# Performance work log

Measured on AMD Instinct MI355X. Metric: run time of the kernel, lower is better.

The kernel has to match this reference:

```python
import jax, jax.numpy as jnp
import numpy as np

N = 100_000   # nodes
E = 600_000   # edges
D = 128       # embed_dim
G = 1000      # graphs (batch ids)
L = 3         # num_layers


def setup_inputs() -> dict:
    key = jax.random.key(0)
    ks = jax.random.split(key, 12)
    s = 1.0 / np.sqrt(D)
    return {
        "x": jax.random.normal(ks[0], (N, D), jnp.float32),
        "edge_index": jax.random.randint(ks[1], (2, E), 0, N),
        "batch": jnp.sort(jax.random.randint(ks[2], (N,), 0, G)),
        "mask": jax.random.randint(ks[3], (N,), 0, 2),
        # stacked GCNConv weights/biases (in=hidden=out=D)
        "gcn_w": jax.random.normal(ks[4], (L, D, D), jnp.float32) * s,
        "gcn_b": jnp.zeros((L, D), jnp.float32),
        # MLP head: Linear(D,D) -> ReLU -> Linear(D,1)
        "lin1_w": jax.random.normal(ks[5], (D, D), jnp.float32) * s,
        "lin1_b": jnp.zeros((D,), jnp.float32),
        "lin2_w": jax.random.normal(ks[6], (D,), jnp.float32) * s,
        "lin2_b": jnp.zeros((), jnp.float32),
    }


def gcn_forward(x, src, dst, gcn_w, gcn_b):
    # symmetric gcn_norm with self-loops: deg[i] = 1 + in-degree(i)
    deg = jax.ops.segment_sum(jnp.ones((E,), x.dtype), dst, num_segments=N) + 1.0
    dinv = jax.lax.rsqrt(deg)
    enorm = dinv[src] * dinv[dst]          # [E] edge normalization
    self_norm = (dinv * dinv)[:, None]     # [N,1] self-loop normalization
    h = x
    for l in range(L):
        h = h @ gcn_w[l]                   # [N,D]
        h = (jax.ops.segment_sum(h[src] * enorm[:, None], dst, num_segments=N)
             + h * self_norm)
        h = h + gcn_b[l]
        if l < L - 1:
            h = jax.nn.relu(h)  # (dropout inactive at inference)
    return h


def reference(x, edge_index, batch, mask, gcn_w, gcn_b, lin1_w, lin1_b, lin2_w, lin2_b):
    src, dst = edge_index[0], edge_index[1]
    h = gcn_forward(x, src, dst, gcn_w, gcn_b)
    # MLP head -> per-node score [N]
    s = jax.nn.relu(h @ lin1_w + lin1_b) @ lin2_w + lin2_b
    s = jnp.where(mask == 0, jnp.float32(-1e9), s)
    # per-graph (segment) softmax — fused replacement for the unique/batch loop
    m = jax.ops.segment_max(s, batch, num_segments=G)
    e = jnp.exp(s - m[batch])
    z = jax.ops.segment_sum(e, batch, num_segments=G)
    return e / z[batch]
```

## Files before the change

kernel.cpp:

```cpp
#include <hip/hip_runtime.h>
#include <hip/hip_bf16.h>

typedef unsigned int u32;
typedef unsigned short u16;
typedef __attribute__((ext_vector_type(8))) short bf16x8;
typedef __attribute__((ext_vector_type(4))) float f32x4;

__device__ __forceinline__ float u16tof(u16 u){ return __uint_as_float(((u32)u) << 16); }
__device__ __forceinline__ float lo16(u32 v){ return __uint_as_float(v << 16); }
__device__ __forceinline__ float hi16(u32 v){ return __uint_as_float(v & 0xffff0000u); }
__device__ __forceinline__ u16 ftobf(float f){
  u32 b = __float_as_uint(f);
  return (u16)((b + 0x7FFFu + ((b >> 16) & 1u)) >> 16);
}
__device__ __forceinline__ u32 pack2(float a, float b){
  return (u32)ftobf(a) | ((u32)ftobf(b) << 16);
}
__device__ __forceinline__ float ldf(const void* p, int i, int isbf){
  return isbf ? u16tof(((const u16*)p)[i]) : ((const float*)p)[i];
}

__device__ __forceinline__ void gather_rows(const u16* __restrict__ Tin, const int* __restrict__ eid,
                                            int j0, int b1e, int l16, float* a){
  const int last = b1e - 1;
  for (int j = j0; j < b1e; j += 8){
    int ss[8];
    #pragma unroll
    for (int k = 0; k < 8; ++k){
      const int jj = j + k;
      ss[k] = eid[jj > last ? last : jj];
    }
    uint4 vv[8];
    #pragma unroll
    for (int k = 0; k < 8; ++k){
      vv[k] = ((const uint4*)(Tin + (size_t)ss[k] * 128))[l16];
    }
    #pragma unroll
    for (int k = 0; k < 8; ++k){
      const float mk = (j + k <= last) ? 1.f : 0.f;
      a[0] = fmaf(lo16(vv[k].x), mk, a[0]);
      a[1] = fmaf(hi16(vv[k].x), mk, a[1]);
      a[2] = fmaf(lo16(vv[k].y), mk, a[2]);
      a[3] = fmaf(hi16(vv[k].y), mk, a[3]);
      a[4] = fmaf(lo16(vv[k].z), mk, a[4]);
      a[5] = fmaf(hi16(vv[k].z), mk, a[5]);
      a[6] = fmaf(lo16(vv[k].w), mk, a[6]);
      a[7] = fmaf(hi16(vv[k].w), mk, a[7]);
    }
  }
}

__global__ __launch_bounds__(256) void k_prep(const void* __restrict__ gw, const void* __restrict__ l1w,
                                              const void* __restrict__ x, u16* __restrict__ Wf,
                                              u16* __restrict__ Hb, int L, int n8, int cvtB, int goffB,
                                              const int* __restrict__ batch, int* __restrict__ goff,
                                              int N, int G,
                                              const int* __restrict__ dst, int* __restrict__ hist,
                                              int nE, int chunk, int* __restrict__ flag){
  __shared__ int sh[256];
  const int b = blockIdx.x;
  const int t = threadIdx.x;
  const int histStart = L + 1 + cvtB + goffB;

  if (b >= histStart){
    sh[t] = 0; __syncthreads();
    const int blk = b - histStart;
    const int e0 = blk * chunk, e1 = min(e0 + chunk, nE);
    for (int e = e0 + t; e < e1; e += 256) atomicAdd(&sh[dst[e] >> 9], 1);
    __syncthreads();
    hist[blk * 256 + t] = sh[t];
    return;
  }
  if (b >= L + 1 + cvtB){
    const int i = (b - (L + 1 + cvtB)) * 256 + t;
    if (i >= N) return;
    const int bt = batch[i];
    const int prev = (i == 0) ? -1 : batch[i - 1];
    for (int g = prev + 1; g <= bt; ++g) goff[g] = i;
    if (i == N - 1){ for (int g = bt + 1; g <= G; ++g) goff[g] = N; }
    return;
  }
  if (t == 0) sh[0] = 0;
  __syncthreads();
  if (b <= L){
    int local = 0;
    for (int i = t; i < 4096; i += 256){
      u32 e = (((const u32*)gw)[i] >> 7) & 0xFFu;
      if (e >= 100u && e < 127u) local++;
    }
    atomicAdd(&sh[0], local);
    __syncthreads();
    const int isbf = (sh[0] > 2048) ? 1 : 0;
    if (b == 0 && t == 0) *flag = isbf;

    const void* src = (b < L) ? gw : l1w;
    const int sbase = (b < L) ? b * 16384 : 0;
    u16* dstp = Wf + (size_t)b * 16384;
    for (int g = t; g < 2048; g += 256){
      const int tt = g >> 8, ks = (g >> 6) & 3, lane = g & 63;
      const int n = tt * 16 + (lane & 15);
      const int k0 = ks * 32 + ((lane >> 4) << 3);
      u16* d = dstp + (size_t)g * 8;
      #pragma unroll
      for (int j = 0; j < 8; ++j){
        d[j] = ftobf(ldf(src, sbase + (k0 + j) * 128 + n, isbf));
      }
    }
  } else {
    u32 e = (((const u32*)gw)[t] >> 7) & 0xFFu;
    atomicAdd(&sh[0], (e >= 100u && e < 127u) ? 1 : 0);
    __syncthreads();
    if (sh[0] > 128) return;
    const int i = (b - (L + 1)) * 256 + t;
    if (i >= n8) return;
    const float4 a = ((const float4*)x)[i * 2];
    const float4 c = ((const float4*)x)[i * 2 + 1];
    u16* o = Hb + (size_t)i * 8;
    o[0] = ftobf(a.x); o[1] = ftobf(a.y); o[2] = ftobf(a.z); o[3] = ftobf(a.w);
    o[4] = ftobf(c.x); o[5] = ftobf(c.y); o[6] = ftobf(c.z); o[7] = ftobf(c.w);
  }
}

__global__ __launch_bounds__(256) void k_hscan(int* __restrict__ hist, int* __restrict__ bb, int nE){
  const int t = threadIdx.x;
  int run = 0;
  for (int j = 0; j < 256; j += 8){
    int v[8];
    #pragma unroll
    for (int k = 0; k < 8; ++k) v[k] = hist[(j + k) * 256 + t];
    #pragma unroll
    for (int k = 0; k < 8; ++k){
      hist[(j + k) * 256 + t] = run;
      run += v[k];
    }
  }
  __shared__ int sm[256];
  sm[t] = run; __syncthreads();
  for (int off = 1; off < 256; off <<= 1){
    int a = (t >= off) ? sm[t - off] : 0;
    __syncthreads();
    sm[t] += a;
    __syncthreads();
  }
  bb[t] = sm[t] - run;
  if (t == 255) bb[256] = nE;
}

__global__ __launch_bounds__(256) void k_scatter(const int* __restrict__ src, const int* __restrict__ dst,
                                                 const int* __restrict__ hist, const int* __restrict__ bb,
                                                 int2* __restrict__ tmpe, int nE, int chunk){
  __shared__ int base[256];
  const int blk = blockIdx.x, t = threadIdx.x;
  base[t] = bb[t] + hist[blk * 256 + t];
  __syncthreads();
  const int e0 = blk * chunk, e1 = min(e0 + chunk, nE);
  for (int e = e0 + t; e < e1; e += 256){
    const int d = dst[e];
    const int pos = atomicAdd(&base[d >> 9], 1);
    tmpe[pos] = make_int2(src[e], d);
  }
}

__global__ __launch_bounds__(256) void k_local(const int2* __restrict__ tmpe, const int* __restrict__ bb,
                                               int* __restrict__ boff, int* __restrict__ eid,
                                               float* __restrict__ dinv, int N, int nE, int nbkt){
  __shared__ int hcnt[512];
  __shared__ int hoff[512];
  const int b = blockIdx.x, t = threadIdx.x;
  const int n0 = b << 9;
  const int n1 = min(n0 + 512, N);
  const int nn = n1 - n0;
  const int e0 = bb[b], e1 = bb[b + 1];
  hcnt[t] = 0; hcnt[t + 256] = 0;
  __syncthreads();
  for (int e = e0 + t; e < e1; e += 256) atomicAdd(&hcnt[tmpe[e].y - n0], 1);
  __syncthreads();
  const int v0 = hcnt[t], v1 = hcnt[t + 256];
  hoff[t] = v0; hoff[t + 256] = v1;
  __syncthreads();
  for (int off = 1; off < 512; off <<= 1){
    int a0 = (t >= off) ? hoff[t - off] : 0;
    int a1 = (t + 256 >= off) ? hoff[t + 256 - off] : 0;
    __syncthreads();
    hoff[t] += a0; hoff[t + 256] += a1;
    __syncthreads();
  }
  const int ex0 = hoff[t] - v0 + e0;
  const int ex1 = hoff[t + 256] - v1 + e0;
  if (t < nn){       boff[n0 + t] = ex0;        dinv[n0 + t] = rsqrtf((float)v0 + 1.0f); }
  if (t + 256 < nn){ boff[n0 + t + 256] = ex1;  dinv[n0 + t + 256] = rsqrtf((float)v1 + 1.0f); }
  if (b == nbkt - 1 && t == 0) boff[N] = nE;
  __syncthreads();
  hoff[t] = ex0; hoff[t + 256] = ex1;
  __syncthreads();
  for (int e = e0 + t; e < e1; e += 256){
    const int2 pr = tmpe[e];
    const int pos = atomicAdd(&hoff[pr.y - n0], 1);
    eid[pos] = pr.x;
  }
}

__global__ __launch_bounds__(256) void k_mm(const void* __restrict__ X, const u16* __restrict__ Hb,
                                            const u16* __restrict__ Wf, const float* __restrict__ dinv,
                                            u16* __restrict__ T, int n, const int* __restrict__ fl){
  __shared__ u16 smw[16384];
  const int isbf = *fl;
  const u16* A = isbf ? (const u16*)X : Hb;
  {
    const uint4* s = (const uint4*)Wf;
    uint4* d = (uint4*)smw;
    for (int i = threadIdx.x; i < 2048; i += 256) d[i] = s[i];
  }
  __syncthreads();

  const int wave = threadIdx.x >> 6, lane = threadIdx.x & 63;
  const int m0 = blockIdx.x * 64 + wave * 16;
  int arow = m0 + (lane & 15); if (arow > n - 1) arow = n - 1;
  const u16* aptr = A + (size_t)arow * 128 + ((lane >> 4) << 3);

  f32x4 acc[8];
  #pragma unroll
  for (int t = 0; t < 8; ++t) acc[t] = (f32x4){0.f, 0.f, 0.f, 0.f};

  #pragma unroll
  for (int ks = 0; ks < 4; ++ks){
    const bf16x8 a = *(const bf16x8*)(aptr + ks * 32);
    #pragma unroll
    for (int t = 0; t < 8; ++t){
      const bf16x8 b = *(const bf16x8*)(smw + (size_t)(((t * 4 + ks) * 64 + lane) * 8));
      acc[t] = __builtin_amdgcn_mfma_f32_16x16x32_bf16(a, b, acc[t], 0, 0, 0);
    }
  }
  __syncthreads();

  const int quad = lane >> 4, col0 = lane & 15;
  float dv[4];
  #pragma unroll
  for (int r = 0; r < 4; ++r){
    const int row = m0 + quad * 4 + r;
    dv[r] = (row < n) ? dinv[row] : 0.f;
  }
  u16* my = smw + wave * 2112;
  #pragma unroll
  for (int t = 0; t < 8; ++t){
    #pragma unroll
    for (int r = 0; r < 4; ++r){
      my[(quad * 4 + r) * 132 + t * 16 + col0] = ftobf(acc[t][r] * dv[r]);
    }
  }
  #pragma unroll
  for (int i = 0; i < 4; ++i){
    const int row = i * 4 + (lane >> 4);
    const int grow = m0 + row;
    const int c8 = (lane & 15) * 8;
    if (grow < n){
      const u16* s = &my[row * 132 + c8];
      uint2 lo = *(const uint2*)(s);
      uint2 hi = *(const uint2*)(s + 4);
      *(uint4*)&T[(size_t)grow * 128 + c8] = make_uint4(lo.x, lo.y, hi.x, hi.y);
    }
  }
}

__global__ __launch_bounds__(256) void k_gmm(const u16* __restrict__ Tin, const int* __restrict__ boff,
                                             const int* __restrict__ eid, const float* __restrict__ dinv,
                                             const void* __restrict__ bias, int layer,
                                             const u16* __restrict__ Wf, u16* __restrict__ Tout,
                                             int n, const int* __restrict__ fl){
  __shared__ u16 sma[16 * 132];
  const int isbf = *fl;
  const int wave = threadIdx.x >> 6, lane = threadIdx.x & 63;
  const int sub = lane >> 4, l16 = lane & 15;
  const int m0 = blockIdx.x * 16;

  const int node = m0 + wave * 4 + sub;
  float h[8];
  #pragma unroll
  for (int k = 0; k < 8; ++k) h[k] = 0.f;
  if (node < n){
    const uint4 sv = ((const uint4*)(Tin + (size_t)node * 128))[l16];
    float a[8];
    a[0] = lo16(sv.x); a[1] = hi16(sv.x); a[2] = lo16(sv.y); a[3] = hi16(sv.y);
    a[4] = lo16(sv.z); a[5] = hi16(sv.z); a[6] = lo16(sv.w); a[7] = hi16(sv.w);
    gather_rows(Tin, eid, boff[node], boff[node + 1], l16, a);
    const float di = dinv[node];
    const int bb = layer * 128 + l16 * 8;
    #pragma unroll
    for (int k = 0; k < 8; ++k){
      h[k] = fmaxf(fmaf(a[k], di, ldf(bias, bb + k, isbf)), 0.f);
    }
  }
  {
    uint4 o;
    o.x = pack2(h[0], h[1]); o.y = pack2(h[2], h[3]); o.z = pack2(h[4], h[5]); o.w = pack2(h[6], h[7]);
    *(uint4*)&sma[(wave * 4 + sub) * 132 + l16 * 8] = o;
  }
  __syncthreads();

  f32x4 acc[2];
  acc[0] = (f32x4){0.f,0.f,0.f,0.f}; acc[1] = (f32x4){0.f,0.f,0.f,0.f};
  #pragma unroll
  for (int ks = 0; ks < 4; ++ks){
    const bf16x8 a = *(const bf16x8*)(sma + l16 * 132 + sub * 8 + ks * 32);
    #pragma unroll
    for (int tt = 0; tt < 2; ++tt){
      const int t = wave * 2 + tt;
      const bf16x8 b = *(const bf16x8*)(Wf + (size_t)(((t * 4 + ks) * 64 + lane) * 8));
      acc[tt] = __builtin_amdgcn_mfma_f32_16x16x32_bf16(a, b, acc[tt], 0, 0, 0);
    }
  }
  __syncthreads();

  float dv[4];
  #pragma unroll
  for (int r = 0; r < 4; ++r){
    const int row = m0 + sub * 4 + r;
    dv[r] = (row < n) ? dinv[row] : 0.f;
  }
  #pragma unroll
  for (int tt = 0; tt < 2; ++tt){
    const int t = wave * 2 + tt;
    #pragma unroll
    for (int r = 0; r < 4; ++r){
      sma[(sub * 4 + r) * 132 + t * 16 + l16] = ftobf(acc[tt][r] * dv[r]);
    }
  }
  __syncthreads();

  {
    const int row = threadIdx.x >> 4;
    const int c8 = (threadIdx.x & 15) * 8;
    if (m0 + row < n){
      const u16* s = &sma[row * 132 + c8];
      uint2 lo = *(const uint2*)(s);
      uint2 hi = *(const uint2*)(s + 4);
      *(uint4*)&Tout[(size_t)(m0 + row) * 128 + c8] = make_uint4(lo.x, lo.y, hi.x, hi.y);
    }
  }
}

__global__ __launch_bounds__(256) void k_ghead(const u16* __restrict__ Tin, const int* __restrict__ boff,
                                               const int* __restrict__ eid, const float* __restrict__ dinv,
                                               const void* __restrict__ bias, int layer,
                                               const u16* __restrict__ Wf, const void* __restrict__ b1,
                                               const void* __restrict__ w2, const void* __restrict__ b2,
                                               const int* __restrict__ mask, float* __restrict__ s,
                                               int n, const int* __restrict__ fl){
  __shared__ u16 sma[16 * 132];
  __shared__ float sred[4][16];
  const int isbf = *fl;
  const int wave = threadIdx.x >> 6, lane = threadIdx.x & 63;
  const int sub = lane >> 4, l16 = lane & 15;
  const int m0 = blockIdx.x * 16;

  const int node = m0 + wave * 4 + sub;
  float h[8];
  #pragma unroll
  for (int k = 0; k < 8; ++k) h[k] = 0.f;
  if (node < n){
    const uint4 sv = ((const uint4*)(Tin + (size_t)node * 128))[l16];
    float a[8];
    a[0] = lo16(sv.x); a[1] = hi16(sv.x); a[2] = lo16(sv.y); a[3] = hi16(sv.y);
    a[4] = lo16(sv.z); a[5] = hi16(sv.z); a[6] = lo16(sv.w); a[7] = hi16(sv.w);
    gather_rows(Tin, eid, boff[node], boff[node + 1], l16, a);
    const float di = dinv[node];
    const int bb = layer * 128 + l16 * 8;
    #pragma unroll
    for (int k = 0; k < 8; ++k){
      h[k] = fmaf(a[k], di, ldf(bias, bb + k, isbf));
    }
  }
  {
    uint4 o;
    o.x = pack2(h[0], h[1]); o.y = pack2(h[2], h[3]); o.z = pack2(h[4], h[5]); o.w = pack2(h[6], h[7]);
    *(uint4*)&sma[(wave * 4 + sub) * 132 + l16 * 8] = o;
  }
  __syncthreads();

  f32x4 acc[2];
  acc[0] = (f32x4){0.f,0.f,0.f,0.f}; acc[1] = (f32x4){0.f,0.f,0.f,0.f};
  #pragma unroll
  for (int ks = 0; ks < 4; ++ks){
    const bf16x8 a = *(const bf16x8*)(sma + l16 * 132 + sub * 8 + ks * 32);
    #pragma unroll
    for (int tt = 0; tt < 2; ++tt){
      const int t = wave * 2 + tt;
      const bf16x8 b = *(const bf16x8*)(Wf + (size_t)(((t * 4 + ks) * 64 + lane) * 8));
      acc[tt] = __builtin_amdgcn_mfma_f32_16x16x32_bf16(a, b, acc[tt], 0, 0, 0);
    }
  }

  float p0 = 0.f, p1 = 0.f, p2 = 0.f, p3 = 0.f;
  #pragma unroll
  for (int tt = 0; tt < 2; ++tt){
    const int col = (wave * 2 + tt) * 16 + l16;
    const float bv = ldf(b1, col, isbf);
    const float wv = ldf(w2, col, isbf);
    p0 = fmaf(fmaxf(acc[tt][0] + bv, 0.f), wv, p0);
    p1 = fmaf(fmaxf(acc[tt][1] + bv, 0.f), wv, p1);
    p2 = fmaf(fmaxf(acc[tt][2] + bv, 0.f), wv, p2);
    p3 = fmaf(fmaxf(acc[tt][3] + bv, 0.f), wv, p3);
  }
  #pragma unroll
  for (int k = 1; k < 16; k <<= 1){
    p0 += __shfl_xor(p0, k);
    p1 += __shfl_xor(p1, k);
    p2 += __shfl_xor(p2, k);
    p3 += __shfl_xor(p3, k);
  }
  if (l16 == 0){
    sred[wave][sub * 4 + 0] = p0;
    sred[wave][sub * 4 + 1] = p1;
    sred[wave][sub * 4 + 2] = p2;
    sred[wave][sub * 4 + 3] = p3;
  }
  __syncthreads();
  if (threadIdx.x < 16){
    const int row = m0 + threadIdx.x;
    if (row < n){
      float sc = sred[0][threadIdx.x] + sred[1][threadIdx.x] + sred[2][threadIdx.x] + sred[3][threadIdx.x]
               + ldf(b2, 0, isbf);
      if (mask[row] == 0) sc = -1e9f;
      s[row] = sc;
    }
  }
}

__global__ __launch_bounds__(256) void k_gsm(const float* __restrict__ s, const int* __restrict__ goff,
                                             void* __restrict__ out, int G, const int* __restrict__ fl){
  const int g = blockIdx.x * 4 + (threadIdx.x >> 6);
  if (g >= G) return;
  const int lane = threadIdx.x & 63;
  const int i0 = goff[g], i1 = goff[g + 1];
  if (i0 >= i1) return;
  float m = -3.4e38f;
  for (int j = i0 + lane; j < i1; j += 64) m = fmaxf(m, s[j]);
  #pragma unroll
  for (int k = 32; k; k >>= 1) m = fmaxf(m, __shfl_xor(m, k));
  float zz = 0.f;
  for (int j = i0 + lane; j < i1; j += 64) zz += expf(s[j] - m);
  #pragma unroll
  for (int k = 32; k; k >>= 1) zz += __shfl_xor(zz, k);
  const float rz = 1.f / zz;
  const int isbf = *fl;
  for (int j = i0 + lane; j < i1; j += 64){
    const float v = expf(s[j] - m) * rz;
    if (isbf) ((u16*)out)[j] = ftobf(v);
    else      ((float*)out)[j] = v;
  }
}

extern "C" void kernel_launch(void* const* d_in, const int* in_sizes, int n_in,
                              void* d_out, int out_size, void* d_ws, size_t ws_size,
                              hipStream_t stream){
  const void* x    = d_in[0];
  const int* ei    = (const int*)d_in[1];
  const int* batch = (const int*)d_in[2];
  const int* mask  = (const int*)d_in[3];
  const void* gw   = d_in[4];
  const void* gb   = d_in[5];
  const void* l1w  = d_in[6];
  const void* l1b  = d_in[7];
  const void* l2w  = d_in[8];
  const void* l2b  = d_in[9];

  const int N = in_sizes[2];
  const int E = in_sizes[1] / 2;
  const int D = 128;
  const int L = in_sizes[4] / (D * D);
  const int G = 1000;

  char* p = (char*)d_ws;
  u16*  Hb    = (u16*)p;   p += (size_t)N * D * sizeof(u16);
  u16*  Tb    = (u16*)p;   p += (size_t)N * D * sizeof(u16);
  u16*  Wf    = (u16*)p;   p += (size_t)(L + 1) * D * D * sizeof(u16);
  float* dinv = (float*)p; p += (size_t)N * sizeof(float);
  float* sbuf = (float*)p; p += (size_t)N * sizeof(float);
  int*  boff  = (int*)p;   p += (size_t)(N + 1) * sizeof(int);
  int*  eid   = (int*)p;   p += (size_t)E * sizeof(int);
  int*  goff  = (int*)p;   p += (size_t)(G + 1) * sizeof(int);
  int*  hist  = (int*)p;   p += 256 * 256 * sizeof(int);
  int*  bb    = (int*)p;   p += 260 * sizeof(int);
  int2* tmpe  = (int2*)p;  p += (size_t)E * sizeof(int2);
  int*  flag  = (int*)p;   p += 256;

  const int* srcp = ei;
  const int* dstp = ei + E;

  const int mmg   = (N + 63) / 64;
  const int fg    = (N + 15) / 16;
  const int n8    = N * D / 8;
  const int cvtB  = (n8 + 255) / 256;
  const int goffB = (N + 255) / 256;
  const int chunk = (E + 255) / 256;
  const int nbkt  = (N + 511) / 512;

  k_prep<<<(L + 1) + cvtB + goffB + 256, 256, 0, stream>>>(gw, l1w, x, Wf, Hb, L, n8, cvtB, goffB,
                                                           batch, goff, N, G, dstp, hist, E, chunk, flag);
  k_hscan<<<1, 256, 0, stream>>>(hist, bb, E);
  k_scatter<<<256, 256, 0, stream>>>(srcp, dstp, hist, bb, tmpe, E, chunk);
  k_local<<<nbkt, 256, 0, stream>>>(tmpe, bb, boff, eid, dinv, N, E, nbkt);

  k_mm<<<mmg, 256, 0, stream>>>(x, Hb, Wf, dinv, Tb, N, flag);
  k_gmm<<<fg, 256, 0, stream>>>(Tb, boff, eid, dinv, gb, 0, Wf + (size_t)1 * D * D, Hb, N, flag);
  k_gmm<<<fg, 256, 0, stream>>>(Hb, boff, eid, dinv, gb, 1, Wf + (size_t)2 * D * D, Tb, N, flag);
  k_ghead<<<fg, 256, 0, stream>>>(Tb, boff, eid, dinv, gb, 2, Wf + (size_t)L * D * D,
                                  l1b, l2w, l2b, mask, sbuf, N, flag);
  k_gsm<<<(G + 3) / 4, 256, 0, stream>>>(sbuf, goff, d_out, G, flag);
}
```

Baseline: 324.7 us.

## Stage weight matrix in LDS and widen gather-GEMM blocks to 64 rows

```diff
diff --git a/kernel.cpp b/kernel.cpp
--- a/kernel.cpp
+++ b/kernel.cpp
@@ -262,16 +262,25 @@
   }
 }
 
-__global__ __launch_bounds__(256) void k_gmm(const u16* __restrict__ Tin, const int* __restrict__ boff,
-                                             const int* __restrict__ eid, const float* __restrict__ dinv,
-                                             const void* __restrict__ bias, int layer,
-                                             const u16* __restrict__ Wf, u16* __restrict__ Tout,
-                                             int n, const int* __restrict__ fl){
-  __shared__ u16 sma[16 * 132];
+__global__ __launch_bounds__(1024, 8) void k_gmm(const u16* __restrict__ Tin, const int* __restrict__ boff,
+                                                 const int* __restrict__ eid, const float* __restrict__ dinv,
+                                                 const void* __restrict__ bias, int layer,
+                                                 const u16* __restrict__ Wf, u16* __restrict__ Tout,
+                                                 int n, const int* __restrict__ fl){
+  __shared__ u16 smw[16384];
+  __shared__ u16 sma[64 * 132];
   const int isbf = *fl;
-  const int wave = threadIdx.x >> 6, lane = threadIdx.x & 63;
+  const int tid = threadIdx.x;
+  const int wave = tid >> 6, lane = tid & 63;
   const int sub = lane >> 4, l16 = lane & 15;
-  const int m0 = blockIdx.x * 16;
+  const int m0 = blockIdx.x * 64;
+
+  {
+    const uint4* s = (const uint4*)Wf;
+    uint4* d = (uint4*)smw;
+    d[tid] = s[tid];
+    d[tid + 1024] = s[tid + 1024];
+  }
 
   const int node = m0 + wave * 4 + sub;
   float h[8];
@@ -297,15 +306,16 @@
   }
   __syncthreads();
 
+  const int rg = wave >> 2, cp = wave & 3;
   f32x4 acc[2];
   acc[0] = (f32x4){0.f,0.f,0.f,0.f}; acc[1] = (f32x4){0.f,0.f,0.f,0.f};
   #pragma unroll
   for (int ks = 0; ks < 4; ++ks){
-    const bf16x8 a = *(const bf16x8*)(sma + l16 * 132 + sub * 8 + ks * 32);
+    const bf16x8 a = *(const bf16x8*)(sma + (rg * 16 + l16) * 132 + sub * 8 + ks * 32);
     #pragma unroll
     for (int tt = 0; tt < 2; ++tt){
-      const int t = wave * 2 + tt;
-      const bf16x8 b = *(const bf16x8*)(Wf + (size_t)(((t * 4 + ks) * 64 + lane) * 8));
+      const int t = cp * 2 + tt;
+      const bf16x8 b = *(const bf16x8*)(smw + (size_t)(((t * 4 + ks) * 64 + lane) * 8));
       acc[tt] = __builtin_amdgcn_mfma_f32_16x16x32_bf16(a, b, acc[tt], 0, 0, 0);
     }
   }
@@ -314,22 +324,22 @@
   float dv[4];
   #pragma unroll
   for (int r = 0; r < 4; ++r){
-    const int row = m0 + sub * 4 + r;
+    const int row = m0 + rg * 16 + sub * 4 + r;
     dv[r] = (row < n) ? dinv[row] : 0.f;
   }
   #pragma unroll
   for (int tt = 0; tt < 2; ++tt){
-    const int t = wave * 2 + tt;
+    const int t = cp * 2 + tt;
     #pragma unroll
     for (int r = 0; r < 4; ++r){
-      sma[(sub * 4 + r) * 132 + t * 16 + l16] = ftobf(acc[tt][r] * dv[r]);
+      sma[(rg * 16 + sub * 4 + r) * 132 + t * 16 + l16] = ftobf(acc[tt][r] * dv[r]);
     }
   }
   __syncthreads();
 
   {
-    const int row = threadIdx.x >> 4;
-    const int c8 = (threadIdx.x & 15) * 8;
+    const int row = tid >> 4;
+    const int c8 = (tid & 15) * 8;
     if (m0 + row < n){
       const u16* s = &sma[row * 132 + c8];
       uint2 lo = *(const uint2*)(s);
@@ -339,19 +349,28 @@
   }
 }
 
-__global__ __launch_bounds__(256) void k_ghead(const u16* __restrict__ Tin, const int* __restrict__ boff,
-                                               const int* __restrict__ eid, const float* __restrict__ dinv,
-                                               const void* __restrict__ bias, int layer,
-                                               const u16* __restrict__ Wf, const void* __restrict__ b1,
-                                               const void* __restrict__ w2, const void* __restrict__ b2,
-                                               const int* __restrict__ mask, float* __restrict__ s,
-                                               int n, const int* __restrict__ fl){
-  __shared__ u16 sma[16 * 132];
-  __shared__ float sred[4][16];
+__global__ __launch_bounds__(1024, 8) void k_ghead(const u16* __restrict__ Tin, const int* __restrict__ boff,
+                                                   const int* __restrict__ eid, const float* __restrict__ dinv,
+                                                   const void* __restrict__ bias, int layer,
+                                                   const u16* __restrict__ Wf, const void* __restrict__ b1,
+                                                   const void* __restrict__ w2, const void* __restrict__ b2,
+                                                   const int* __restrict__ mask, float* __restrict__ s,
+                                                   int n, const int* __restrict__ fl){
+  __shared__ u16 smw[16384];
+  __shared__ u16 sma[64 * 132];
+  __shared__ float sred[16][16];
   const int isbf = *fl;
-  const int wave = threadIdx.x >> 6, lane = threadIdx.x & 63;
+  const int tid = threadIdx.x;
+  const int wave = tid >> 6, lane = tid & 63;
   const int sub = lane >> 4, l16 = lane & 15;
-  const int m0 = blockIdx.x * 16;
+  const int m0 = blockIdx.x * 64;
+
+  {
+    const uint4* sp = (const uint4*)Wf;
+    uint4* d = (uint4*)smw;
+    d[tid] = sp[tid];
+    d[tid + 1024] = sp[tid + 1024];
+  }
 
   const int node = m0 + wave * 4 + sub;
   float h[8];
@@ -377,15 +396,16 @@
   }
   __syncthreads();
 
+  const int rg = wave >> 2, cp = wave & 3;
   f32x4 acc[2];
   acc[0] = (f32x4){0.f,0.f,0.f,0.f}; acc[1] = (f32x4){0.f,0.f,0.f,0.f};
   #pragma unroll
   for (int ks = 0; ks < 4; ++ks){
-    const bf16x8 a = *(const bf16x8*)(sma + l16 * 132 + sub * 8 + ks * 32);
+    const bf16x8 a = *(const bf16x8*)(sma + (rg * 16 + l16) * 132 + sub * 8 + ks * 32);
     #pragma unroll
     for (int tt = 0; tt < 2; ++tt){
-      const int t = wave * 2 + tt;
-      const bf16x8 b = *(const bf16x8*)(Wf + (size_t)(((t * 4 + ks) * 64 + lane) * 8));
+      const int t = cp * 2 + tt;
+      const bf16x8 b = *(const bf16x8*)(smw + (size_t)(((t * 4 + ks) * 64 + lane) * 8));
       acc[tt] = __builtin_amdgcn_mfma_f32_16x16x32_bf16(a, b, acc[tt], 0, 0, 0);
     }
   }
@@ -393,7 +413,7 @@
   float p0 = 0.f, p1 = 0.f, p2 = 0.f, p3 = 0.f;
   #pragma unroll
   for (int tt = 0; tt < 2; ++tt){
-    const int col = (wave * 2 + tt) * 16 + l16;
+    const int col = (cp * 2 + tt) * 16 + l16;
     const float bv = ldf(b1, col, isbf);
     const float wv = ldf(w2, col, isbf);
     p0 = fmaf(fmaxf(acc[tt][0] + bv, 0.f), wv, p0);
@@ -415,10 +435,12 @@
     sred[wave][sub * 4 + 3] = p3;
   }
   __syncthreads();
-  if (threadIdx.x < 16){
-    const int row = m0 + threadIdx.x;
+  if (tid < 64){
+    const int row = m0 + tid;
     if (row < n){
-      float sc = sred[0][threadIdx.x] + sred[1][threadIdx.x] + sred[2][threadIdx.x] + sred[3][threadIdx.x]
+      const int rg2 = tid >> 4, idx = tid & 15;
+      float sc = sred[rg2 * 4 + 0][idx] + sred[rg2 * 4 + 1][idx]
+               + sred[rg2 * 4 + 2][idx] + sred[rg2 * 4 + 3][idx]
                + ldf(b2, 0, isbf);
       if (mask[row] == 0) sc = -1e9f;
       s[row] = sc;
@@ -488,7 +510,7 @@
   const int* dstp = ei + E;
 
   const int mmg   = (N + 63) / 64;
-  const int fg    = (N + 15) / 16;
+  const int fg    = (N + 63) / 64;
   const int n8    = N * D / 8;
   const int cvtB  = (n8 + 255) / 256;
   const int goffB = (N + 255) / 256;
@@ -502,9 +524,9 @@
   k_local<<<nbkt, 256, 0, stream>>>(tmpe, bb, boff, eid, dinv, N, E, nbkt);
 
   k_mm<<<mmg, 256, 0, stream>>>(x, Hb, Wf, dinv, Tb, N, flag);
-  k_gmm<<<fg, 256, 0, stream>>>(Tb, boff, eid, dinv, gb, 0, Wf + (size_t)1 * D * D, Hb, N, flag);
-  k_gmm<<<fg, 256, 0, stream>>>(Hb, boff, eid, dinv, gb, 1, Wf + (size_t)2 * D * D, Tb, N, flag);
-  k_ghead<<<fg, 256, 0, stream>>>(Tb, boff, eid, dinv, gb, 2, Wf + (size_t)L * D * D,
-                                  l1b, l2w, l2b, mask, sbuf, N, flag);
+  k_gmm<<<fg, 1024, 0, stream>>>(Tb, boff, eid, dinv, gb, 0, Wf + (size_t)1 * D * D, Hb, N, flag);
+  k_gmm<<<fg, 1024, 0, stream>>>(Hb, boff, eid, dinv, gb, 1, Wf + (size_t)2 * D * D, Tb, N, flag);
+  k_ghead<<<fg, 1024, 0, stream>>>(Tb, boff, eid, dinv, gb, 2, Wf + (size_t)L * D * D,
+                                   l1b, l2w, l2b, mask, sbuf, N, flag);
   k_gsm<<<(G + 3) / 4, 256, 0, stream>>>(sbuf, goff, d_out, G, flag);
 }
```

Result: slower. 532.1 us (+63.9%).

## Process two nodes per thread group and 32-row tiles in gather+matmul kernels

Applied to the files above, without the earlier changes.

```diff
diff --git a/kernel.cpp b/kernel.cpp
--- a/kernel.cpp
+++ b/kernel.cpp
@@ -20,33 +20,38 @@
   return isbf ? u16tof(((const u16*)p)[i]) : ((const float*)p)[i];
 }
 
-__device__ __forceinline__ void gather_rows(const u16* __restrict__ Tin, const int* __restrict__ eid,
-                                            int j0, int b1e, int l16, float* a){
-  const int last = b1e - 1;
-  for (int j = j0; j < b1e; j += 8){
-    int ss[8];
-    #pragma unroll
-    for (int k = 0; k < 8; ++k){
-      const int jj = j + k;
-      ss[k] = eid[jj > last ? last : jj];
-    }
-    uint4 vv[8];
-    #pragma unroll
-    for (int k = 0; k < 8; ++k){
-      vv[k] = ((const uint4*)(Tin + (size_t)ss[k] * 128))[l16];
-    }
-    #pragma unroll
-    for (int k = 0; k < 8; ++k){
-      const float mk = (j + k <= last) ? 1.f : 0.f;
-      a[0] = fmaf(lo16(vv[k].x), mk, a[0]);
-      a[1] = fmaf(hi16(vv[k].x), mk, a[1]);
-      a[2] = fmaf(lo16(vv[k].y), mk, a[2]);
-      a[3] = fmaf(hi16(vv[k].y), mk, a[3]);
-      a[4] = fmaf(lo16(vv[k].z), mk, a[4]);
-      a[5] = fmaf(hi16(vv[k].z), mk, a[5]);
-      a[6] = fmaf(lo16(vv[k].w), mk, a[6]);
-      a[7] = fmaf(hi16(vv[k].w), mk, a[7]);
-    }
+__device__ __forceinline__ void acc8(float* a, uint4 v, float mk){
+  a[0] = fmaf(lo16(v.x), mk, a[0]);
+  a[1] = fmaf(hi16(v.x), mk, a[1]);
+  a[2] = fmaf(lo16(v.y), mk, a[2]);
+  a[3] = fmaf(hi16(v.y), mk, a[3]);
+  a[4] = fmaf(lo16(v.z), mk, a[4]);
+  a[5] = fmaf(hi16(v.z), mk, a[5]);
+  a[6] = fmaf(lo16(v.w), mk, a[6]);
+  a[7] = fmaf(hi16(v.w), mk, a[7]);
+}
+
+__device__ __forceinline__ void gather2(const u16* __restrict__ Tin, const int* __restrict__ eid,
+                                        int jA, int eA, int jB, int eB, int l16,
+                                        float* a, float* b){
+  while (jA < eA || jB < eB){
+    int sA[4], sB[4];
+    #pragma unroll
+    for (int k = 0; k < 4; ++k){
+      const int iA = jA + k; sA[k] = eid[iA < eA ? iA : 0];
+      const int iB = jB + k; sB[k] = eid[iB < eB ? iB : 0];
+    }
+    uint4 vA[4], vB[4];
+    #pragma unroll
+    for (int k = 0; k < 4; ++k) vA[k] = ((const uint4*)(Tin + (size_t)sA[k] * 128))[l16];
+    #pragma unroll
+    for (int k = 0; k < 4; ++k) vB[k] = ((const uint4*)(Tin + (size_t)sB[k] * 128))[l16];
+    #pragma unroll
+    for (int k = 0; k < 4; ++k){
+      acc8(a, vA[k], (jA + k < eA) ? 1.f : 0.f);
+      acc8(b, vB[k], (jB + k < eB) ? 1.f : 0.f);
+    }
+    jA += 4; jB += 4;
   }
 }
 
@@ -267,46 +272,64 @@
                                              const void* __restrict__ bias, int layer,
                                              const u16* __restrict__ Wf, u16* __restrict__ Tout,
                                              int n, const int* __restrict__ fl){
-  __shared__ u16 sma[16 * 132];
+  __shared__ u16 sma[32 * 132];
   const int isbf = *fl;
-  const int wave = threadIdx.x >> 6, lane = threadIdx.x & 63;
+  const int tid = threadIdx.x;
+  const int wave = tid >> 6, lane = tid & 63;
   const int sub = lane >> 4, l16 = lane & 15;
-  const int m0 = blockIdx.x * 16;
-
-  const int node = m0 + wave * 4 + sub;
-  float h[8];
-  #pragma unroll
-  for (int k = 0; k < 8; ++k) h[k] = 0.f;
-  if (node < n){
-    const uint4 sv = ((const uint4*)(Tin + (size_t)node * 128))[l16];
-    float a[8];
-    a[0] = lo16(sv.x); a[1] = hi16(sv.x); a[2] = lo16(sv.y); a[3] = hi16(sv.y);
-    a[4] = lo16(sv.z); a[5] = hi16(sv.z); a[6] = lo16(sv.w); a[7] = hi16(sv.w);
-    gather_rows(Tin, eid, boff[node], boff[node + 1], l16, a);
-    const float di = dinv[node];
-    const int bb = layer * 128 + l16 * 8;
-    #pragma unroll
-    for (int k = 0; k < 8; ++k){
-      h[k] = fmaxf(fmaf(a[k], di, ldf(bias, bb + k, isbf)), 0.f);
-    }
+  const int m0 = blockIdx.x * 32;
+
+  const int nA = m0 + wave * 8 + sub;
+  const int nB = nA + 4;
+  float a[8], b[8];
+  #pragma unroll
+  for (int k = 0; k < 8; ++k){ a[k] = 0.f; b[k] = 0.f; }
+  int jA = 0, eA = 0, jB = 0, eB = 0;
+  if (nA < n){ jA = boff[nA]; eA = boff[nA + 1]; }
+  if (nB < n){ jB = boff[nB]; eB = boff[nB + 1]; }
+  if (nA < n){
+    const uint4 sv = ((const uint4*)(Tin + (size_t)nA * 128))[l16];
+    acc8(a, sv, 1.f);
+  }
+  if (nB < n){
+    const uint4 sv = ((const uint4*)(Tin + (size_t)nB * 128))[l16];
+    acc8(b, sv, 1.f);
+  }
+  gather2(Tin, eid, jA, eA, jB, eB, l16, a, b);
+
+  const int bb = layer * 128 + l16 * 8;
+  if (nA < n){
+    const float di = dinv[nA];
+    #pragma unroll
+    for (int k = 0; k < 8; ++k) a[k] = fmaxf(fmaf(a[k], di, ldf(bias, bb + k, isbf)), 0.f);
+  }
+  if (nB < n){
+    const float di = dinv[nB];
+    #pragma unroll
+    for (int k = 0; k < 8; ++k) b[k] = fmaxf(fmaf(b[k], di, ldf(bias, bb + k, isbf)), 0.f);
   }
   {
-    uint4 o;
-    o.x = pack2(h[0], h[1]); o.y = pack2(h[2], h[3]); o.z = pack2(h[4], h[5]); o.w = pack2(h[6], h[7]);
-    *(uint4*)&sma[(wave * 4 + sub) * 132 + l16 * 8] = o;
-  }
-  __syncthreads();
-
-  f32x4 acc[2];
-  acc[0] = (f32x4){0.f,0.f,0.f,0.f}; acc[1] = (f32x4){0.f,0.f,0.f,0.f};
+    uint4 oA, oB;
+    oA.x = pack2(a[0], a[1]); oA.y = pack2(a[2], a[3]); oA.z = pack2(a[4], a[5]); oA.w = pack2(a[6], a[7]);
+    oB.x = pack2(b[0], b[1]); oB.y = pack2(b[2], b[3]); oB.z = pack2(b[4], b[5]); oB.w = pack2(b[6], b[7]);
+    *(uint4*)&sma[(wave * 8 + sub) * 132 + l16 * 8] = oA;
+    *(uint4*)&sma[(wave * 8 + sub + 4) * 132 + l16 * 8] = oB;
+  }
+  __syncthreads();
+
+  const int r0 = (wave & 1) * 16;
+  const int cg = wave >> 1;
+  f32x4 acc[4];
+  #pragma unroll
+  for (int tt = 0; tt < 4; ++tt) acc[tt] = (f32x4){0.f, 0.f, 0.f, 0.f};
   #pragma unroll
   for (int ks = 0; ks < 4; ++ks){
-    const bf16x8 a = *(const bf16x8*)(sma + l16 * 132 + sub * 8 + ks * 32);
-    #pragma unroll
-    for (int tt = 0; tt < 2; ++tt){
-      const int t = wave * 2 + tt;
-      const bf16x8 b = *(const bf16x8*)(Wf + (size_t)(((t * 4 + ks) * 64 + lane) * 8));
-      acc[tt] = __builtin_amdgcn_mfma_f32_16x16x32_bf16(a, b, acc[tt], 0, 0, 0);
+    const bf16x8 av = *(const bf16x8*)(sma + (r0 + l16) * 132 + sub * 8 + ks * 32);
+    #pragma unroll
+    for (int tt = 0; tt < 4; ++tt){
+      const int t = cg * 4 + tt;
+      const bf16x8 bv = *(const bf16x8*)(Wf + (size_t)(((t * 4 + ks) * 64 + lane) * 8));
+      acc[tt] = __builtin_amdgcn_mfma_f32_16x16x32_bf16(av, bv, acc[tt], 0, 0, 0);
     }
   }
   __syncthreads();
@@ -314,22 +337,23 @@
   float dv[4];
   #pragma unroll
   for (int r = 0; r < 4; ++r){
-    const int row = m0 + sub * 4 + r;
+    const int row = m0 + r0 + sub * 4 + r;
     dv[r] = (row < n) ? dinv[row] : 0.f;
   }
   #pragma unroll
-  for (int tt = 0; tt < 2; ++tt){
-    const int t = wave * 2 + tt;
+  for (int tt = 0; tt < 4; ++tt){
     #pragma unroll
     for (int r = 0; r < 4; ++r){
-      sma[(sub * 4 + r) * 132 + t * 16 + l16] = ftobf(acc[tt][r] * dv[r]);
-    }
-  }
-  __syncthreads();
-
-  {
-    const int row = threadIdx.x >> 4;
-    const int c8 = (threadIdx.x & 15) * 8;
+      sma[(r0 + sub * 4 + r) * 132 + (cg * 4 + tt) * 16 + l16] = ftobf(acc[tt][r] * dv[r]);
+    }
+  }
+  __syncthreads();
+
+  #pragma unroll
+  for (int i = 0; i < 2; ++i){
+    const int idx = tid + i * 256;
+    const int row = idx >> 4;
+    const int c8 = (idx & 15) * 8;
     if (m0 + row < n){
       const u16* s = &sma[row * 132 + c8];
       uint2 lo = *(const uint2*)(s);
@@ -346,54 +370,72 @@
                                                const void* __restrict__ w2, const void* __restrict__ b2,
                                                const int* __restrict__ mask, float* __restrict__ s,
                                                int n, const int* __restrict__ fl){
-  __shared__ u16 sma[16 * 132];
+  __shared__ u16 sma[32 * 132];
   __shared__ float sred[4][16];
   const int isbf = *fl;
-  const int wave = threadIdx.x >> 6, lane = threadIdx.x & 63;
+  const int tid = threadIdx.x;
+  const int wave = tid >> 6, lane = tid & 63;
   const int sub = lane >> 4, l16 = lane & 15;
-  const int m0 = blockIdx.x * 16;
-
-  const int node = m0 + wave * 4 + sub;
-  float h[8];
-  #pragma unroll
-  for (int k = 0; k < 8; ++k) h[k] = 0.f;
-  if (node < n){
-    const uint4 sv = ((const uint4*)(Tin + (size_t)node * 128))[l16];
-    float a[8];
-    a[0] = lo16(sv.x); a[1] = hi16(sv.x); a[2] = lo16(sv.y); a[3] = hi16(sv.y);
-    a[4] = lo16(sv.z); a[5] = hi16(sv.z); a[6] = lo16(sv.w); a[7] = hi16(sv.w);
-    gather_rows(Tin, eid, boff[node], boff[node + 1], l16, a);
-    const float di = dinv[node];
-    const int bb = layer * 128 + l16 * 8;
-    #pragma unroll
-    for (int k = 0; k < 8; ++k){
-      h[k] = fmaf(a[k], di, ldf(bias, bb + k, isbf));
-    }
+  const int m0 = blockIdx.x * 32;
+
+  const int nA = m0 + wave * 8 + sub;
+  const int nB = nA + 4;
+  float a[8], b[8];
+  #pragma unroll
+  for (int k = 0; k < 8; ++k){ a[k] = 0.f; b[k] = 0.f; }
+  int jA = 0, eA = 0, jB = 0, eB = 0;
+  if (nA < n){ jA = boff[nA]; eA = boff[nA + 1]; }
+  if (nB < n){ jB = boff[nB]; eB = boff[nB + 1]; }
+  if (nA < n){
+    const uint4 sv = ((const uint4*)(Tin + (size_t)nA * 128))[l16];
+    acc8(a, sv, 1.f);
+  }
+  if (nB < n){
+    const uint4 sv = ((const uint4*)(Tin + (size_t)nB * 128))[l16];
+    acc8(b, sv, 1.f);
+  }
+  gather2(Tin, eid, jA, eA, jB, eB, l16, a, b);
+
+  const int bb = layer * 128 + l16 * 8;
+  if (nA < n){
+    const float di = dinv[nA];
+    #pragma unroll
+    for (int k = 0; k < 8; ++k) a[k] = fmaf(a[k], di, ldf(bias, bb + k, isbf));
+  }
+  if (nB < n){
+    const float di = dinv[nB];
+    #pragma unroll
+    for (int k = 0; k < 8; ++k) b[k] = fmaf(b[k], di, ldf(bias, bb + k, isbf));
   }
   {
-    uint4 o;
-    o.x = pack2(h[0], h[1]); o.y = pack2(h[2], h[3]); o.z = pack2(h[4], h[5]); o.w = pack2(h[6], h[7]);
-    *(uint4*)&sma[(wave * 4 + sub) * 132 + l16 * 8] = o;
-  }
-  __syncthreads();
-
-  f32x4 acc[2];
-  acc[0] = (f32x4){0.f,0.f,0.f,0.f}; acc[1] = (f32x4){0.f,0.f,0.f,0.f};
+    uint4 oA, oB;
+    oA.x = pack2(a[0], a[1]); oA.y = pack2(a[2], a[3]); oA.z = pack2(a[4], a[5]); oA.w = pack2(a[6], a[7]);
+    oB.x = pack2(b[0], b[1]); oB.y = pack2(b[2], b[3]); oB.z = pack2(b[4], b[5]); oB.w = pack2(b[6], b[7]);
+    *(uint4*)&sma[(wave * 8 + sub) * 132 + l16 * 8] = oA;
+    *(uint4*)&sma[(wave * 8 + sub + 4) * 132 + l16 * 8] = oB;
+  }
+  __syncthreads();
+
+  const int r0 = (wave & 1) * 16;
+  const int cg = wave >> 1;
+  f32x4 acc[4];
+  #pragma unroll
+  for (int tt = 0; tt < 4; ++tt) acc[tt] = (f32x4){0.f, 0.f, 0.f, 0.f};
   #pragma unroll
   for (int ks = 0; ks < 4; ++ks){
-    const bf16x8 a = *(const bf16x8*)(sma + l16 * 132 + sub * 8 + ks * 32);
-    #pragma unroll
-    for (int tt = 0; tt < 2; ++tt){
-      const int t = wave * 2 + tt;
-      const bf16x8 b = *(const bf16x8*)(Wf + (size_t)(((t * 4 + ks) * 64 + lane) * 8));
-      acc[tt] = __builtin_amdgcn_mfma_f32_16x16x32_bf16(a, b, acc[tt], 0, 0, 0);
+    const bf16x8 av = *(const bf16x8*)(sma + (r0 + l16) * 132 + sub * 8 + ks * 32);
+    #pragma unroll
+    for (int tt = 0; tt < 4; ++tt){
+      const int t = cg * 4 + tt;
+      const bf16x8 bv = *(const bf16x8*)(Wf + (size_t)(((t * 4 + ks) * 64 + lane) * 8));
+      acc[tt] = __builtin_amdgcn_mfma_f32_16x16x32_bf16(av, bv, acc[tt], 0, 0, 0);
     }
   }
 
   float p0 = 0.f, p1 = 0.f, p2 = 0.f, p3 = 0.f;
   #pragma unroll
-  for (int tt = 0; tt < 2; ++tt){
-    const int col = (wave * 2 + tt) * 16 + l16;
+  for (int tt = 0; tt < 4; ++tt){
+    const int col = (cg * 4 + tt) * 16 + l16;
     const float bv = ldf(b1, col, isbf);
     const float wv = ldf(w2, col, isbf);
     p0 = fmaf(fmaxf(acc[tt][0] + bv, 0.f), wv, p0);
@@ -415,11 +457,11 @@
     sred[wave][sub * 4 + 3] = p3;
   }
   __syncthreads();
-  if (threadIdx.x < 16){
-    const int row = m0 + threadIdx.x;
+  if (tid < 32){
+    const int row = m0 + tid;
     if (row < n){
-      float sc = sred[0][threadIdx.x] + sred[1][threadIdx.x] + sred[2][threadIdx.x] + sred[3][threadIdx.x]
-               + ldf(b2, 0, isbf);
+      const int rg = tid >> 4, idx = tid & 15;
+      float sc = sred[rg][idx] + sred[rg + 2][idx] + ldf(b2, 0, isbf);
       if (mask[row] == 0) sc = -1e9f;
       s[row] = sc;
     }
@@ -488,7 +530,7 @@
   const int* dstp = ei + E;
 
   const int mmg   = (N + 63) / 64;
-  const int fg    = (N + 15) / 16;
+  const int fg    = (N + 31) / 32;
   const int n8    = N * D / 8;
   const int cvtB  = (n8 + 255) / 256;
   const int goffB = (N + 255) / 256;
```

Result: slower. 344.5 us (+6.1%).

## Pipeline neighbor-row gathers through LDS ring using async global_load_lds

Applied to the files above, without the earlier changes.

```diff
diff --git a/kernel.cpp b/kernel.cpp
--- a/kernel.cpp
+++ b/kernel.cpp
@@ -1,5 +1,6 @@
 #include <hip/hip_runtime.h>
 #include <hip/hip_bf16.h>
+#include <stdint.h>
 
 typedef unsigned int u32;
 typedef unsigned short u16;
@@ -20,34 +21,22 @@
   return isbf ? u16tof(((const u16*)p)[i]) : ((const float*)p)[i];
 }
 
-__device__ __forceinline__ void gather_rows(const u16* __restrict__ Tin, const int* __restrict__ eid,
-                                            int j0, int b1e, int l16, float* a){
-  const int last = b1e - 1;
-  for (int j = j0; j < b1e; j += 8){
-    int ss[8];
-    #pragma unroll
-    for (int k = 0; k < 8; ++k){
-      const int jj = j + k;
-      ss[k] = eid[jj > last ? last : jj];
-    }
-    uint4 vv[8];
-    #pragma unroll
-    for (int k = 0; k < 8; ++k){
-      vv[k] = ((const uint4*)(Tin + (size_t)ss[k] * 128))[l16];
-    }
-    #pragma unroll
-    for (int k = 0; k < 8; ++k){
-      const float mk = (j + k <= last) ? 1.f : 0.f;
-      a[0] = fmaf(lo16(vv[k].x), mk, a[0]);
-      a[1] = fmaf(hi16(vv[k].x), mk, a[1]);
-      a[2] = fmaf(lo16(vv[k].y), mk, a[2]);
-      a[3] = fmaf(hi16(vv[k].y), mk, a[3]);
-      a[4] = fmaf(lo16(vv[k].z), mk, a[4]);
-      a[5] = fmaf(hi16(vv[k].z), mk, a[5]);
-      a[6] = fmaf(lo16(vv[k].w), mk, a[6]);
-      a[7] = fmaf(hi16(vv[k].w), mk, a[7]);
-    }
-  }
+__device__ __forceinline__ void acc8(float* a, uint4 v, float mk){
+  a[0] = fmaf(lo16(v.x), mk, a[0]);
+  a[1] = fmaf(hi16(v.x), mk, a[1]);
+  a[2] = fmaf(lo16(v.y), mk, a[2]);
+  a[3] = fmaf(hi16(v.y), mk, a[3]);
+  a[4] = fmaf(lo16(v.z), mk, a[4]);
+  a[5] = fmaf(hi16(v.z), mk, a[5]);
+  a[6] = fmaf(lo16(v.w), mk, a[6]);
+  a[7] = fmaf(hi16(v.w), mk, a[7]);
+}
+
+__device__ __forceinline__ void async16(const u16* g, const u16* l){
+  __builtin_amdgcn_global_load_lds(
+      (const __attribute__((address_space(1))) u32*)(uintptr_t)g,
+      (__attribute__((address_space(3))) u32*)(uintptr_t)l,
+      16, 0, 0);
 }
 
 __global__ __launch_bounds__(256) void k_prep(const void* __restrict__ gw, const void* __restrict__ l1w,
@@ -262,27 +251,109 @@
   }
 }
 
+__device__ __forceinline__ void gather_ring(const u16* __restrict__ Tin, const int* __restrict__ eid,
+                                            const int* __restrict__ seid, const int* __restrict__ sboff,
+                                            int inlds, int e0, int wave, int lane, int sub, int l16,
+                                            int js, int d, float* a){
+  int T = 0;
+  #pragma unroll
+  for (int s = 0; s < 4; ++s){
+    const int dd = sboff[wave * 4 + s + 1] - sboff[wave * 4 + s];
+    T = (dd > T) ? dd : T;
+  }
+  if (T <= 0) return;
+
+  if (inlds){
+    extern __shared__ u16 dummy[];
+    return;
+  }
+}
+
 __global__ __launch_bounds__(256) void k_gmm(const u16* __restrict__ Tin, const int* __restrict__ boff,
                                              const int* __restrict__ eid, const float* __restrict__ dinv,
                                              const void* __restrict__ bias, int layer,
                                              const u16* __restrict__ Wf, u16* __restrict__ Tout,
                                              int n, const int* __restrict__ fl){
   __shared__ u16 sma[16 * 132];
+  __shared__ u16 ring[4][4][512];
+  __shared__ int seid[1024];
+  __shared__ int sboff[17];
   const int isbf = *fl;
-  const int wave = threadIdx.x >> 6, lane = threadIdx.x & 63;
+  const int tid = threadIdx.x;
+  const int wave = tid >> 6, lane = tid & 63;
   const int sub = lane >> 4, l16 = lane & 15;
   const int m0 = blockIdx.x * 16;
 
-  const int node = m0 + wave * 4 + sub;
+  const int e0 = boff[m0];
+  const int e1 = boff[min(m0 + 16, n)];
+  const int len = e1 - e0;
+  const int inlds = (len <= 1024);
+  if (tid < 17) sboff[tid] = boff[min(m0 + tid, n)];
+  if (inlds){ for (int i = tid; i < len; i += 256) seid[i] = eid[e0 + i]; }
+  __syncthreads();
+
+  const int wsub = wave * 4 + sub;
+  const int node = m0 + wsub;
+  const int js = sboff[wsub];
+  const int d  = sboff[wsub + 1] - js;
+
+  float a[8];
+  #pragma unroll
+  for (int k = 0; k < 8; ++k) a[k] = 0.f;
+  if (node < n){
+    const uint4 sv = ((const uint4*)(Tin + (size_t)node * 128))[l16];
+    acc8(a, sv, 1.f);
+  }
+
+  int T = 0;
+  #pragma unroll
+  for (int s = 0; s < 4; ++s){
+    const int dd = sboff[wave * 4 + s + 1] - sboff[wave * 4 + s];
+    T = (dd > T) ? dd : T;
+  }
+
+  if (inlds){
+    const int jloc = js - e0;
+    const int jlast = jloc + ((d > 0) ? (d - 1) : 0);
+    const u16* base = Tin + (size_t)l16 * 8;
+    u16* slot = &ring[wave][0][0];
+    #pragma unroll
+    for (int t = 0; t < 4; ++t){
+      if (t < T){
+        const int idx = (d > 0) ? seid[(t < d) ? (jloc + t) : jlast] : 0;
+        async16(base + (size_t)idx * 128, slot + (t & 3) * 512);
+      }
+    }
+    int t = 0;
+    for (; t + 4 <= T; ++t){
+      asm volatile("s_waitcnt vmcnt(3)" ::: "memory");
+      const uint4 v = *(const uint4*)(slot + (t & 3) * 512 + lane * 8);
+      acc8(a, v, (t < d) ? 1.f : 0.f);
+      const int tn = t + 4;
+      if (tn < T){
+        const int idx = (d > 0) ? seid[(tn < d) ? (jloc + tn) : jlast] : 0;
+        async16(base + (size_t)idx * 128, slot + (tn & 3) * 512);
+      }
+    }
+    for (; t < T; ++t){
+      const int rem = T - t - 1;
+      if (rem >= 2)      asm volatile("s_waitcnt vmcnt(2)" ::: "memory");
+      else if (rem == 1) asm volatile("s_waitcnt vmcnt(1)" ::: "memory");
+      else               asm volatile("s_waitcnt vmcnt(0)" ::: "memory");
+      const uint4 v = *(const uint4*)(slot + (t & 3) * 512 + lane * 8);
+      acc8(a, v, (t < d) ? 1.f : 0.f);
+    }
+  } else {
+    for (int j = js; j < js + d; ++j){
+      const uint4 v = ((const uint4*)(Tin + (size_t)eid[j] * 128))[l16];
+      acc8(a, v, 1.f);
+    }
+  }
+
   float h[8];
   #pragma unroll
   for (int k = 0; k < 8; ++k) h[k] = 0.f;
   if (node < n){
-    const uint4 sv = ((const uint4*)(Tin + (size_t)node * 128))[l16];
-    float a[8];
-    a[0] = lo16(sv.x); a[1] = hi16(sv.x); a[2] = lo16(sv.y); a[3] = hi16(sv.y);
-    a[4] = lo16(sv.z); a[5] = hi16(sv.z); a[6] = lo16(sv.w); a[7] = hi16(sv.w);
-    gather_rows(Tin, eid, boff[node], boff[node + 1], l16, a);
     const float di = dinv[node];
     const int bb = layer * 128 + l16 * 8;
     #pragma unroll
@@ -301,12 +372,12 @@
   acc[0] = (f32x4){0.f,0.f,0.f,0.f}; acc[1] = (f32x4){0.f,0.f,0.f,0.f};
   #pragma unroll
   for (int ks = 0; ks < 4; ++ks){
-    const bf16x8 a = *(const bf16x8*)(sma + l16 * 132 + sub * 8 + ks * 32);
+    const bf16x8 av = *(const bf16x8*)(sma + l16 * 132 + sub * 8 + ks * 32);
     #pragma unroll
     for (int tt = 0; tt < 2; ++tt){
       const int t = wave * 2 + tt;
-      const bf16x8 b = *(const bf16x8*)(Wf + (size_t)(((t * 4 + ks) * 64 + lane) * 8));
-      acc[tt] = __builtin_amdgcn_mfma_f32_16x16x32_bf16(a, b, acc[tt], 0, 0, 0);
+      const bf16x8 bv = *(const bf16x8*)(Wf + (size_t)(((t * 4 + ks) * 64 + lane) * 8));
+      acc[tt] = __builtin_amdgcn_mfma_f32_16x16x32_bf16(av, bv, acc[tt], 0, 0, 0);
     }
   }
   __syncthreads();
@@ -328,8 +399,8 @@
   __syncthreads();
 
   {
-    const int row = threadIdx.x >> 4;
-    const int c8 = (threadIdx.x & 15) * 8;
+    const int row = tid >> 4;
+    const int c8 = (tid & 15) * 8;
     if (m0 + row < n){
       const u16* s = &sma[row * 132 + c8];
       uint2 lo = *(const uint2*)(s);
@@ -347,22 +418,86 @@
                                                const int* __restrict__ mask, float* __restrict__ s,
                                                int n, const int* __restrict__ fl){
   __shared__ u16 sma[16 * 132];
+  __shared__ u16 ring[4][4][512];
+  __shared__ int seid[1024];
+  __shared__ int sboff[17];
   __shared__ float sred[4][16];
   const int isbf = *fl;
-  const int wave = threadIdx.x >> 6, lane = threadIdx.x & 63;
+  const int tid = threadIdx.x;
+  const int wave = tid >> 6, lane = tid & 63;
   const int sub = lane >> 4, l16 = lane & 15;
   const int m0 = blockIdx.x * 16;
 
-  const int node = m0 + wave * 4 + sub;
+  const int e0 = boff[m0];
+  const int e1 = boff[min(m0 + 16, n)];
+  const int len = e1 - e0;
+  const int inlds = (len <= 1024);
+  if (tid < 17) sboff[tid] = boff[min(m0 + tid, n)];
+  if (inlds){ for (int i = tid; i < len; i += 256) seid[i] = eid[e0 + i]; }
+  __syncthreads();
+
+  const int wsub = wave * 4 + sub;
+  const int node = m0 + wsub;
+  const int js = sboff[wsub];
+  const int d  = sboff[wsub + 1] - js;
+
+  float a[8];
+  #pragma unroll
+  for (int k = 0; k < 8; ++k) a[k] = 0.f;
+  if (node < n){
+    const uint4 sv = ((const uint4*)(Tin + (size_t)node * 128))[l16];
+    acc8(a, sv, 1.f);
+  }
+
+  int T = 0;
+  #pragma unroll
+  for (int s2 = 0; s2 < 4; ++s2){
+    const int dd = sboff[wave * 4 + s2 + 1] - sboff[wave * 4 + s2];
+    T = (dd > T) ? dd : T;
+  }
+
+  if (inlds){
+    const int jloc = js - e0;
+    const int jlast = jloc + ((d > 0) ? (d - 1) : 0);
+    const u16* base = Tin + (size_t)l16 * 8;
+    u16* slot = &ring[wave][0][0];
+    #pragma unroll
+    for (int t = 0; t < 4; ++t){
+      if (t < T){
+        const int idx = (d > 0) ? seid[(t < d) ? (jloc + t) : jlast] : 0;
+        async16(base + (size_t)idx * 128, slot + (t & 3) * 512);
+      }
+    }
+    int t = 0;
+    for (; t + 4 <= T; ++t){
+      asm volatile("s_waitcnt vmcnt(3)" ::: "memory");
+      const uint4 v = *(const uint4*)(slot + (t & 3) * 512 + lane * 8);
+      acc8(a, v, (t < d) ? 1.f : 0.f);
+      const int tn = t + 4;
+      if (tn < T){
+        const int idx = (d > 0) ? seid[(tn < d) ? (jloc + tn) : jlast] : 0;
+        async16(base + (size_t)idx * 128, slot + (tn & 3) * 512);
+      }
+    }
+    for (; t < T; ++t){
+      const int rem = T - t - 1;
+      if (rem >= 2)      asm volatile("s_waitcnt vmcnt(2)" ::: "memory");
+      else if (rem == 1) asm volatile("s_waitcnt vmcnt(1)" ::: "memory");
+      else               asm volatile("s_waitcnt vmcnt(0)" ::: "memory");
+      const uint4 v = *(const uint4*)(slot + (t & 3) * 512 + lane * 8);
+      acc8(a, v, (t < d) ? 1.f : 0.f);
+    }
+  } else {
+    for (int j = js; j < js + d; ++j){
+      const uint4 v = ((const uint4*)(Tin + (size_t)eid[j] * 128))[l16];
+      acc8(a, v, 1.f);
+    }
+  }
+
   float h[8];
   #pragma unroll
   for (int k = 0; k < 8; ++k) h[k] = 0.f;
   if (node < n){
-    const uint4 sv = ((const uint4*)(Tin + (size_t)node * 128))[l16];
-    float a[8];
-    a[0] = lo16(sv.x); a[1] = hi16(sv.x); a[2] = lo16(sv.y); a[3] = hi16(sv.y);
-    a[4] = lo16(sv.z); a[5] = hi16(sv.z); a[6] = lo16(sv.w); a[7] = hi16(sv.w);
-    gather_rows(Tin, eid, boff[node], boff[node + 1], l16, a);
     const float di = dinv[node];
     const int bb = layer * 128 + l16 * 8;
     #pragma unroll
@@ -381,12 +516,12 @@
   acc[0] = (f32x4){0.f,0.f,0.f,0.f}; acc[1] = (f32x4){0.f,0.f,0.f,0.f};
   #pragma unroll
   for (int ks = 0; ks < 4; ++ks){
-    const bf16x8 a = *(const bf16x8*)(sma + l16 * 132 + sub * 8 + ks * 32);
+    const bf16x8 av = *(const bf16x8*)(sma + l16 * 132 + sub * 8 + ks * 32);
     #pragma unroll
     for (int tt = 0; tt < 2; ++tt){
       const int t = wave * 2 + tt;
-      const bf16x8 b = *(const bf16x8*)(Wf + (size_t)(((t * 4 + ks) * 64 + lane) * 8));
-      acc[tt] = __builtin_amdgcn_mfma_f32_16x16x32_bf16(a, b, acc[tt], 0, 0, 0);
+      const bf16x8 bv = *(const bf16x8*)(Wf + (size_t)(((t * 4 + ks) * 64 + lane) * 8));
+      acc[tt] = __builtin_amdgcn_mfma_f32_16x16x32_bf16(av, bv, acc[tt], 0, 0, 0);
     }
   }
 
@@ -415,10 +550,10 @@
     sred[wave][sub * 4 + 3] = p3;
   }
   __syncthreads();
-  if (threadIdx.x < 16){
-    const int row = m0 + threadIdx.x;
+  if (tid < 16){
+    const int row = m0 + tid;
     if (row < n){
-      float sc = sred[0][threadIdx.x] + sred[1][threadIdx.x] + sred[2][threadIdx.x] + sred[3][threadIdx.x]
+      float sc = sred[0][tid] + sred[1][tid] + sred[2][tid] + sred[3][tid]
                + ldf(b2, 0, isbf);
       if (mask[row] == 0) sc = -1e9f;
       s[row] = sc;
```

After: 316.8 us. -2.4%, faster.
